# Kernel tuning notes

Hardware: AMD Instinct MI355X
Metric: run time of the kernel (lower is better)

Reference implementation:

```python
import jax, jax.numpy as jnp
import numpy as np

N_NODES = 10000
N_EDGES = 160000
T_STEPS = 2
N_SAMPLE = 2
H_DIM = 64
Z_DIM = 32
K_HEADS = 4
N_IN = 4


def setup_inputs() -> dict:
    key = jax.random.key(0)
    ks = jax.random.split(key, 16)
    sc = lambda fan_in: 1.0 / np.sqrt(fan_in).astype(np.float32)
    inp = {}
    inp["inputs"] = jax.random.normal(ks[0], (N_NODES, T_STEPS, N_IN), jnp.float32)
    inp["zA"] = jax.random.normal(ks[1], (N_NODES, N_SAMPLE, Z_DIM), jnp.float32)
    inp["zG"] = jax.random.normal(ks[2], (N_NODES, N_SAMPLE, Z_DIM), jnp.float32)
    inp["src"] = jax.random.randint(ks[3], (N_EDGES,), 0, N_NODES)
    inp["dst"] = jax.random.randint(ks[4], (N_EDGES,), 0, N_NODES)
    # GAT attention projections (K heads, no bias): Linear(z_dim -> h_dim)
    inp["Ws"] = jax.random.normal(ks[5], (K_HEADS, H_DIM, Z_DIM), jnp.float32) * sc(Z_DIM)
    inp["Wd"] = jax.random.normal(ks[6], (K_HEADS, H_DIM, Z_DIM), jnp.float32) * sc(Z_DIM)
    # F2: Linear(2h -> h, no bias), ReLU, Linear(h -> h, no bias)
    inp["F2_w1"] = jax.random.normal(ks[7], (H_DIM, 2 * H_DIM), jnp.float32) * sc(2 * H_DIM)
    inp["F2_w2"] = jax.random.normal(ks[8], (H_DIM, H_DIM), jnp.float32) * sc(H_DIM)
    # F1: Linear(K*h -> h, no bias), ReLU, Linear(h -> h, no bias)
    inp["F1_w1"] = jax.random.normal(ks[9], (H_DIM, K_HEADS * H_DIM), jnp.float32) * sc(K_HEADS * H_DIM)
    inp["F1_w2"] = jax.random.normal(ks[10], (H_DIM, H_DIM), jnp.float32) * sc(H_DIM)
    # x_enc: Linear(n_in -> h) with bias
    inp["xenc_w"] = jax.random.normal(ks[11], (H_DIM, N_IN), jnp.float32) * sc(N_IN)
    inp["xenc_b"] = jnp.zeros((H_DIM,), jnp.float32)
    # out_fc: Linear(h+z -> h), ReLU, Linear(h -> 4)
    inp["out_w1"] = jax.random.normal(ks[12], (H_DIM, H_DIM + Z_DIM), jnp.float32) * sc(H_DIM + Z_DIM)
    inp["out_b1"] = jnp.zeros((H_DIM,), jnp.float32)
    inp["out_w2"] = jax.random.normal(ks[13], (4, H_DIM), jnp.float32) * sc(H_DIM)
    inp["out_b2"] = jnp.zeros((4,), jnp.float32)
    inp["pred_steps"] = 2
    return inp


def reference(inputs, zA, zG, src, dst, Ws, Wd, F2_w1, F2_w2, F1_w1, F1_w2,
              xenc_w, xenc_b, out_w1, out_b1, out_w2, out_b2, pred_steps):
    N, T, _ = inputs.shape
    S = zA.shape[1]
    K = Ws.shape[0]

    # --- edge attention (GAT.attn), computed once per forward ---
    As = jnp.einsum('nsz,khz->nskh', zG, Ws)          # [N, S, K, H]
    Ad = jnp.einsum('nsz,khz->nskh', zG, Wd)
    e = jnp.sum(As[src] * Ad[dst], axis=-1)           # [E, S, K]
    e = jax.nn.leaky_relu(e, 0.01)
    # per-destination softmax over incoming edges (DGL mailbox softmax over dim=1)
    m = jax.ops.segment_max(e, dst, num_segments=N)
    ex = jnp.exp(e - m[dst])
    denom = jax.ops.segment_sum(ex, dst, num_segments=N)
    alpha = ex / denom[dst]                           # [E, S, K]
    deg = jax.ops.segment_sum(jnp.ones((e.shape[0],), e.dtype), dst, num_segments=N)
    deg = jnp.maximum(deg, 1.0)[:, None, None]        # [N, 1, 1]; mean over mailbox dim

    def step(xt):
        xt_enc = xt @ xenc_w.T + xenc_b               # [N, S, H]
        cat = jnp.concatenate([xt_enc[src], xt_enc[dst]], axis=-1)  # [E, S, 2H]
        dA = jax.nn.relu(cat @ F2_w1.T) @ F2_w2.T     # [E, S, H]
        # per-head attention-weighted mean over in-neighbors; loop over K (small, fixed)
        res = [jax.ops.segment_sum(alpha[:, :, k:k + 1] * dA, dst, num_segments=N) / deg
               for k in range(K)]
        res = jnp.concatenate(res, axis=-1)           # [N, S, K*H]
        deltax = jax.nn.relu(res @ F1_w1.T) @ F1_w2.T # [N, S, H]
        h = jnp.concatenate([deltax, zA], axis=-1)    # [N, S, H+Z]
        dx = jax.nn.relu(h @ out_w1.T + out_b1) @ out_w2.T + out_b2  # [N, S, 4]
        return xt + dx

    inp_t = jnp.transpose(inputs, (1, 0, 2))          # [T, N, n_in]
    inp_t = jnp.broadcast_to(inp_t[:, :, None, :], (T, N, S, inp_t.shape[-1]))
    preds = []
    for b in range(0, T, pred_steps):                 # blocks of pred_steps
        xt = inp_t[b]
        for _ in range(pred_steps):
            xt = step(xt)
            preds.append(xt)
    out = jnp.stack(preds, axis=0)                    # [T, N, S, 4]
    return jnp.transpose(out, (1, 0, 2, 3))           # [N, T, S, 4]
```

## Files before the change

### kernel.cpp

```cpp
#include <hip/hip_runtime.h>

#define NN 10000
#define NE 160000
#define TT 2
#define SS 2
#define HH 64
#define ZZ 32
#define KK 4
#define NIN 4

typedef short bf16x8 __attribute__((ext_vector_type(8)));
typedef float f32x4 __attribute__((ext_vector_type(4)));

__device__ __forceinline__ unsigned short f2b(float x) {
    unsigned u = __float_as_uint(x);
    u += 0x7fffu + ((u >> 16) & 1u);
    return (unsigned short)(u >> 16);
}
__device__ __forceinline__ float bf2f(unsigned short u) {
    return __uint_as_float(((unsigned)u) << 16);
}

__device__ __forceinline__ void wave_lds_fence() {
    asm volatile("s_waitcnt lgkmcnt(0)" ::: "memory");
    __builtin_amdgcn_wave_barrier();
}

__device__ __forceinline__ float edge_score(const unsigned* __restrict__ zp,
                                            const float* __restrict__ qf) {
    float a = 0.f;
#pragma unroll
    for (int j = 0; j < 16; ++j) {
        unsigned u = zp[j];
        a += __uint_as_float(u << 16) * qf[2*j]
           + __uint_as_float(u & 0xffff0000u) * qf[2*j+1];
    }
    return a > 0.f ? a : 0.01f*a;
}

__global__ __launch_bounds__(256) void k_prep(
    const float* __restrict__ Ws, const float* __restrict__ Wd,
    const float* __restrict__ F2w1, const float* __restrict__ xw,
    const float* __restrict__ xb, const float* __restrict__ F2w2,
    const float* __restrict__ F1w1, const float* __restrict__ F1w2,
    const float* __restrict__ ow1, const float* __restrict__ ow2,
    const float* __restrict__ zA, const float* __restrict__ zG,
    const float* __restrict__ inputs, const int* __restrict__ dst,
    float* __restrict__ MT, float* __restrict__ G1, float* __restrict__ G2,
    float* __restrict__ c1, float* __restrict__ c2,
    unsigned short* __restrict__ W2b, unsigned short* __restrict__ F1w1b,
    unsigned short* __restrict__ F1w2b, unsigned short* __restrict__ ow1b,
    unsigned short* __restrict__ ow2b, unsigned short* __restrict__ zAb,
    unsigned short* __restrict__ zGb, float* __restrict__ xt,
    int* __restrict__ deg_i)
{
    int b = blockIdx.x;
    int tid = threadIdx.x;
    if (b < 16) {
        int o = b*256 + tid;
        int j = o & 31, i = (o >> 5) & 31, k = o >> 10;
        float acc = 0.0f;
        for (int h = 0; h < HH; ++h)
            acc += Ws[(k*HH + h)*ZZ + i] * Wd[(k*HH + h)*ZZ + j];
        MT[(k*ZZ + j)*ZZ + i] = acc;
    } else if (b == 16) {
        int h = tid >> 2, i = tid & 3;
        float a1 = 0.f, a2 = 0.f;
        for (int j = 0; j < HH; ++j) {
            float x = xw[j*NIN + i];
            a1 += F2w1[h*128 + j] * x;
            a2 += F2w1[h*128 + 64 + j] * x;
        }
        G1[h*4 + i] = a1;
        G2[h*4 + i] = a2;
        if (i == 0) {
            float b1 = 0.f, b2 = 0.f;
            for (int j = 0; j < HH; ++j) {
                float bb = xb[j];
                b1 += F2w1[h*128 + j] * bb;
                b2 += F2w1[h*128 + 64 + j] * bb;
            }
            c1[h] = b1; c2[h] = b2;
        }
    } else {
        int t = (b - 17)*256 + tid;
        if (t < NN*SS*ZZ) { zAb[t] = f2b(zA[t]); zGb[t] = f2b(zG[t]); }
        if (t < HH*HH)    { W2b[t] = f2b(F2w2[t]); F1w2b[t] = f2b(F1w2[t]); }
        if (t < HH*KK*HH) F1w1b[t] = f2b(F1w1[t]);
        if (t < HH*(HH+ZZ)) ow1b[t] = f2b(ow1[t]);
        if (t < 4*HH)     ow2b[t] = f2b(ow2[t]);
        if (t < NN*SS*NIN) {
            int i = t & 3;
            int n = t >> 3;
            xt[t] = inputs[n*(TT*NIN) + i];
        }
        if (t < NE) atomicAdd(deg_i + dst[t], 1);
    }
}

__global__ void k_scan(const int* __restrict__ deg_i, int* __restrict__ offsets,
                       int* __restrict__ cursor) {
    __shared__ int buf0[1024], buf1[1024];
    int tidx = threadIdx.x;
    const int CH = (NN + 1023) / 1024;
    int b0 = tidx * CH;
    int sum = 0;
    for (int i = 0; i < CH; ++i) { int idx = b0 + i; if (idx < NN) sum += deg_i[idx]; }
    buf0[tidx] = sum;
    __syncthreads();
    int* s = buf0; int* d = buf1;
    for (int off = 1; off < 1024; off <<= 1) {
        d[tidx] = s[tidx] + (tidx >= off ? s[tidx - off] : 0);
        __syncthreads();
        int* tmp = s; s = d; d = tmp;
    }
    int run = s[tidx] - sum;
    for (int i = 0; i < CH; ++i) {
        int idx = b0 + i;
        if (idx < NN) { offsets[idx] = run; cursor[idx] = run; run += deg_i[idx]; }
    }
    if (tidx == 0) offsets[NN] = NE;
}

__global__ void k_scatter(const int* __restrict__ src, const int* __restrict__ dst,
                          int* __restrict__ cursor, int* __restrict__ src_by_pos) {
    int e = blockIdx.x * blockDim.x + threadIdx.x;
    if (e >= NE) return;
    int pos = atomicAdd(cursor + dst[e], 1);
    src_by_pos[pos] = src[e];
}

__global__ __launch_bounds__(64) void k_attn_agg0(
    const float* __restrict__ MT, const float* __restrict__ zG,
    const unsigned short* __restrict__ zGb, const int* __restrict__ src_by_pos,
    const int* __restrict__ offsets, const float* __restrict__ xt,
    const float* __restrict__ G1, const float* __restrict__ G2,
    const float* __restrict__ c1, const float* __restrict__ c2,
    float* alpha, unsigned short* __restrict__ agg_b)
{
    __shared__ float sq[132];
    __shared__ float alpha_s[64][4];
    int item = blockIdx.x;
    int n = item >> 1, s = item & 1;
    int l = threadIdx.x;
    int i = l >> 2, k = l & 3;
    int r0 = offsets[n], r1 = offsets[n+1];

    {
        int i0 = l & 31;
        int k0 = l >> 5;
        int k1 = k0 + 2;
        const float* zg = zG + item*ZZ;
        float acc0 = 0.f, acc1 = 0.f;
#pragma unroll
        for (int j = 0; j < ZZ; ++j) {
            float z = zg[j];
            acc0 += MT[(k0*ZZ + j)*ZZ + i0] * z;
            acc1 += MT[(k1*ZZ + j)*ZZ + i0] * z;
        }
        sq[k0*33 + i0] = acc0;
        sq[k1*33 + i0] = acc1;
    }
    wave_lds_fence();
    float qf[32];
#pragma unroll
    for (int j = 0; j < 32; ++j) qf[j] = sq[k*33 + j];

    float E[8];
    float mx = -1e30f;
    int nit = 0;
    for (int idx = r0 + i; idx < r1; idx += 16, ++nit) {
        int sn = src_by_pos[idx];
        float e = edge_score((const unsigned*)(zGb + (sn*SS + s)*ZZ), qf);
        if (nit < 8) E[nit] = e;
        mx = fmaxf(mx, e);
    }
#pragma unroll
    for (int off = 4; off < 64; off <<= 1) mx = fmaxf(mx, __shfl_xor(mx, off));
    float sum = 0.f;
    nit = 0;
    for (int idx = r0 + i; idx < r1; idx += 16, ++nit) {
        float e = (nit < 8) ? E[nit]
                : edge_score((const unsigned*)(zGb + (src_by_pos[idx]*SS + s)*ZZ), qf);
        float ex = __expf(e - mx);
        if (nit < 8) E[nit] = ex;
        sum += ex;
    }
#pragma unroll
    for (int off = 4; off < 64; off <<= 1) sum += __shfl_xor(sum, off);
    int deg = r1 - r0;
    float dd = (float)(deg > 1 ? deg : 1);
    float inv = sum > 0.f ? 1.f/(sum*dd) : 0.f;
    nit = 0;
    for (int idx = r0 + i; idx < r1; idx += 16, ++nit) {
        float a = ((nit < 8) ? E[nit]
                 : __expf(edge_score((const unsigned*)(zGb + (src_by_pos[idx]*SS + s)*ZZ), qf) - mx)) * inv;
        alpha[(idx*2 + s)*4 + k] = a;
        int jo = idx - r0;
        if (jo < 64) alpha_s[jo][k] = a;
    }
    wave_lds_fence();

    int h = l;
    const float4 g1 = *(const float4*)(G1 + h*4);
    const float4 g2 = *(const float4*)(G2 + h*4);
    const float4 xd = *(const float4*)(xt + item*4);
    float p2 = c2[h] + xd.x*g2.x + xd.y*g2.y + xd.z*g2.z + xd.w*g2.w;
    float c1h = c1[h];
    float a0 = 0.f, a1 = 0.f, a2 = 0.f, a3 = 0.f;
    int jo = 0;
    for (; jo + 4 <= deg; jo += 4) {
        int sn0 = src_by_pos[r0 + jo];
        int sn1 = src_by_pos[r0 + jo + 1];
        int sn2 = src_by_pos[r0 + jo + 2];
        int sn3 = src_by_pos[r0 + jo + 3];
        float4 x0 = *(const float4*)(xt + (sn0*SS + s)*NIN);
        float4 x1 = *(const float4*)(xt + (sn1*SS + s)*NIN);
        float4 x2 = *(const float4*)(xt + (sn2*SS + s)*NIN);
        float4 x3 = *(const float4*)(xt + (sn3*SS + s)*NIN);
        float4 w0 = (jo+0 < 64) ? *(const float4*)(&alpha_s[jo+0][0])
                                : *(const float4*)(alpha + ((r0+jo+0)*2 + s)*4);
        float4 w1 = (jo+1 < 64) ? *(const float4*)(&alpha_s[jo+1][0])
                                : *(const float4*)(alpha + ((r0+jo+1)*2 + s)*4);
        float4 w2 = (jo+2 < 64) ? *(const float4*)(&alpha_s[jo+2][0])
                                : *(const float4*)(alpha + ((r0+jo+2)*2 + s)*4);
        float4 w3 = (jo+3 < 64) ? *(const float4*)(&alpha_s[jo+3][0])
                                : *(const float4*)(alpha + ((r0+jo+3)*2 + s)*4);
        float p, hd;
        p = c1h + x0.x*g1.x + x0.y*g1.y + x0.z*g1.z + x0.w*g1.w;
        hd = p + p2; hd = hd > 0.f ? hd : 0.f;
        a0 += w0.x*hd; a1 += w0.y*hd; a2 += w0.z*hd; a3 += w0.w*hd;
        p = c1h + x1.x*g1.x + x1.y*g1.y + x1.z*g1.z + x1.w*g1.w;
        hd = p + p2; hd = hd > 0.f ? hd : 0.f;
        a0 += w1.x*hd; a1 += w1.y*hd; a2 += w1.z*hd; a3 += w1.w*hd;
        p = c1h + x2.x*g1.x + x2.y*g1.y + x2.z*g1.z + x2.w*g1.w;
        hd = p + p2; hd = hd > 0.f ? hd : 0.f;
        a0 += w2.x*hd; a1 += w2.y*hd; a2 += w2.z*hd; a3 += w2.w*hd;
        p = c1h + x3.x*g1.x + x3.y*g1.y + x3.z*g1.z + x3.w*g1.w;
        hd = p + p2; hd = hd > 0.f ? hd : 0.f;
        a0 += w3.x*hd; a1 += w3.y*hd; a2 += w3.z*hd; a3 += w3.w*hd;
    }
    for (; jo < deg; ++jo) {
        int sn = src_by_pos[r0 + jo];
        float4 x0 = *(const float4*)(xt + (sn*SS + s)*NIN);
        float4 w4 = (jo < 64) ? *(const float4*)(&alpha_s[jo][0])
                              : *(const float4*)(alpha + ((r0+jo)*2 + s)*4);
        float p = c1h + x0.x*g1.x + x0.y*g1.y + x0.z*g1.z + x0.w*g1.w;
        float hd = p + p2; hd = hd > 0.f ? hd : 0.f;
        a0 += w4.x*hd; a1 += w4.y*hd; a2 += w4.z*hd; a3 += w4.w*hd;
    }
    agg_b[item*256 +       h] = f2b(a0);
    agg_b[item*256 + 64  + h] = f2b(a1);
    agg_b[item*256 + 128 + h] = f2b(a2);
    agg_b[item*256 + 192 + h] = f2b(a3);
}

__global__ __launch_bounds__(64) void k_agg2(
    const float* __restrict__ xt, const float* __restrict__ G1,
    const float* __restrict__ G2, const float* __restrict__ c1,
    const float* __restrict__ c2, const int* __restrict__ src_by_pos,
    const int* __restrict__ offsets, const float* __restrict__ alpha,
    unsigned short* __restrict__ agg_b)
{
    int item = blockIdx.x;
    int n = item >> 1, s = item & 1;
    int h = threadIdx.x;
    int r0 = offsets[n], r1 = offsets[n+1];
    const float4 g1 = *(const float4*)(G1 + h*4);
    const float4 g2 = *(const float4*)(G2 + h*4);
    const float4 xd = *(const float4*)(xt + item*4);
    float p2 = c2[h] + xd.x*g2.x + xd.y*g2.y + xd.z*g2.z + xd.w*g2.w;
    float c1h = c1[h];
    float a0 = 0.f, a1 = 0.f, a2 = 0.f, a3 = 0.f;
    int idx = r0;
    for (; idx + 4 <= r1; idx += 4) {
        int sn0 = src_by_pos[idx];
        int sn1 = src_by_pos[idx+1];
        int sn2 = src_by_pos[idx+2];
        int sn3 = src_by_pos[idx+3];
        float4 x0 = *(const float4*)(xt + (sn0*SS + s)*NIN);
        float4 x1 = *(const float4*)(xt + (sn1*SS + s)*NIN);
        float4 x2 = *(const float4*)(xt + (sn2*SS + s)*NIN);
        float4 x3 = *(const float4*)(xt + (sn3*SS + s)*NIN);
        float4 w0 = *(const float4*)(alpha + ((idx+0)*2 + s)*4);
        float4 w1 = *(const float4*)(alpha + ((idx+1)*2 + s)*4);
        float4 w2 = *(const float4*)(alpha + ((idx+2)*2 + s)*4);
        float4 w3 = *(const float4*)(alpha + ((idx+3)*2 + s)*4);
        float p, hd;
        p = c1h + x0.x*g1.x + x0.y*g1.y + x0.z*g1.z + x0.w*g1.w;
        hd = p + p2; hd = hd > 0.f ? hd : 0.f;
        a0 += w0.x*hd; a1 += w0.y*hd; a2 += w0.z*hd; a3 += w0.w*hd;
        p = c1h + x1.x*g1.x + x1.y*g1.y + x1.z*g1.z + x1.w*g1.w;
        hd = p + p2; hd = hd > 0.f ? hd : 0.f;
        a0 += w1.x*hd; a1 += w1.y*hd; a2 += w1.z*hd; a3 += w1.w*hd;
        p = c1h + x2.x*g1.x + x2.y*g1.y + x2.z*g1.z + x2.w*g1.w;
        hd = p + p2; hd = hd > 0.f ? hd : 0.f;
        a0 += w2.x*hd; a1 += w2.y*hd; a2 += w2.z*hd; a3 += w2.w*hd;
        p = c1h + x3.x*g1.x + x3.y*g1.y + x3.z*g1.z + x3.w*g1.w;
        hd = p + p2; hd = hd > 0.f ? hd : 0.f;
        a0 += w3.x*hd; a1 += w3.y*hd; a2 += w3.z*hd; a3 += w3.w*hd;
    }
    for (; idx < r1; ++idx) {
        int sn = src_by_pos[idx];
        float4 x0 = *(const float4*)(xt + (sn*SS + s)*NIN);
        float4 w0 = *(const float4*)(alpha + (idx*2 + s)*4);
        float p = c1h + x0.x*g1.x + x0.y*g1.y + x0.z*g1.z + x0.w*g1.w;
        float hd = p + p2; hd = hd > 0.f ? hd : 0.f;
        a0 += w0.x*hd; a1 += w0.y*hd; a2 += w0.z*hd; a3 += w0.w*hd;
    }
    agg_b[item*256 +       h] = f2b(a0);
    agg_b[item*256 + 64  + h] = f2b(a1);
    agg_b[item*256 + 128 + h] = f2b(a2);
    agg_b[item*256 + 192 + h] = f2b(a3);
}

__global__ __launch_bounds__(256) void k_node_mfma(
    const unsigned short* __restrict__ agg_b, const unsigned short* __restrict__ zAb,
    const unsigned short* __restrict__ W2b,
    const unsigned short* __restrict__ F1w1b, const unsigned short* __restrict__ F1w2b,
    const unsigned short* __restrict__ ow1b, const unsigned short* __restrict__ ow2b,
    const float* __restrict__ ob1, const float* __restrict__ ob2,
    float* __restrict__ xt, float* __restrict__ out, int tstep)
{
    __shared__ unsigned short res_s[4][16*264];
    __shared__ unsigned short hid_s[4][16*72];
    __shared__ unsigned short hcat_s[4][16*104];
    int tid = threadIdx.x;
    int w = tid >> 6, l = tid & 63, l15 = l & 15, qq = l >> 4;

    bf16x8 w2f[2][4], b2f[2][4], o1f[3][4], bo2[2];
#pragma unroll
    for (int nb = 0; nb < 4; ++nb) {
        int n = nb*16 + l15;
#pragma unroll
        for (int kb = 0; kb < 2; ++kb) {
            w2f[kb][nb] = *(const bf16x8*)(W2b  + n*64 + kb*32 + qq*8);
            b2f[kb][nb] = *(const bf16x8*)(F1w2b + n*64 + kb*32 + qq*8);
        }
#pragma unroll
        for (int kb = 0; kb < 3; ++kb)
            o1f[kb][nb] = *(const bf16x8*)(ow1b + n*96 + kb*32 + qq*8);
    }
#pragma unroll
    for (int kb = 0; kb < 2; ++kb) {
        if (l15 < 4) bo2[kb] = *(const bf16x8*)(ow2b + l15*64 + kb*32 + qq*8);
        else {
            bf16x8 z;
#pragma unroll
            for (int j = 0; j < 8; ++j) z[j] = 0;
            bo2[kb] = z;
        }
    }
    float b1v[4];
#pragma unroll
    for (int nb = 0; nb < 4; ++nb) b1v[nb] = ob1[nb*16 + l15];
    float b2v = (l15 < 4) ? ob2[l15] : 0.0f;

    int itemBase = blockIdx.x*64 + w*16;
    if (itemBase >= NN*SS) return;

    *(uint4*)(&hcat_s[w][l15*104 + 64 + qq*8]) =
        *(const uint4*)(zAb + (itemBase + l15)*ZZ + qq*8);

#pragma unroll
    for (int k = 0; k < 4; ++k) {
        f32x4 acc0[4];
#pragma unroll
        for (int nb = 0; nb < 4; ++nb) acc0[nb] = (f32x4)(0.0f);
#pragma unroll
        for (int kb = 0; kb < 2; ++kb) {
            bf16x8 af = *(const bf16x8*)(agg_b + (itemBase + l15)*256 + k*64 + kb*32 + qq*8);
#pragma unroll
            for (int nb = 0; nb < 4; ++nb)
                acc0[nb] = __builtin_amdgcn_mfma_f32_16x16x32_bf16(af, w2f[kb][nb], acc0[nb], 0, 0, 0);
        }
#pragma unroll
        for (int nb = 0; nb < 4; ++nb)
#pragma unroll
            for (int r = 0; r < 4; ++r)
                res_s[w][(qq*4 + r)*264 + k*64 + nb*16 + l15] = f2b(acc0[nb][r]);
    }

    f32x4 acc[4];
#pragma unroll
    for (int nb = 0; nb < 4; ++nb) acc[nb] = (f32x4)(0.0f);
#pragma unroll
    for (int kb = 0; kb < 8; ++kb) {
        bf16x8 af = *(const bf16x8*)(&res_s[w][l15*264 + kb*32 + qq*8]);
#pragma unroll
        for (int nb = 0; nb < 4; ++nb) {
            bf16x8 bf = *(const bf16x8*)(F1w1b + (nb*16 + l15)*256 + kb*32 + qq*8);
            acc[nb] = __builtin_amdgcn_mfma_f32_16x16x32_bf16(af, bf, acc[nb], 0, 0, 0);
        }
    }
#pragma unroll
    for (int nb = 0; nb < 4; ++nb)
#pragma unroll
        for (int r = 0; r < 4; ++r) {
            float v = acc[nb][r];
            hid_s[w][(qq*4 + r)*72 + nb*16 + l15] = f2b(v > 0.0f ? v : 0.0f);
        }

    f32x4 acc2[4];
#pragma unroll
    for (int nb = 0; nb < 4; ++nb) acc2[nb] = (f32x4)(0.0f);
#pragma unroll
    for (int kb = 0; kb < 2; ++kb) {
        bf16x8 af = *(const bf16x8*)(&hid_s[w][l15*72 + kb*32 + qq*8]);
#pragma unroll
        for (int nb = 0; nb < 4; ++nb)
            acc2[nb] = __builtin_amdgcn_mfma_f32_16x16x32_bf16(af, b2f[kb][nb], acc2[nb], 0, 0, 0);
    }
#pragma unroll
    for (int nb = 0; nb < 4; ++nb)
#pragma unroll
        for (int r = 0; r < 4; ++r)
            hcat_s[w][(qq*4 + r)*104 + nb*16 + l15] = f2b(acc2[nb][r]);

    f32x4 acc3[4];
#pragma unroll
    for (int nb = 0; nb < 4; ++nb) acc3[nb] = (f32x4)(0.0f);
#pragma unroll
    for (int kb = 0; kb < 3; ++kb) {
        bf16x8 af = *(const bf16x8*)(&hcat_s[w][l15*104 + kb*32 + qq*8]);
#pragma unroll
        for (int nb = 0; nb < 4; ++nb)
            acc3[nb] = __builtin_amdgcn_mfma_f32_16x16x32_bf16(af, o1f[kb][nb], acc3[nb], 0, 0, 0);
    }
#pragma unroll
    for (int nb = 0; nb < 4; ++nb)
#pragma unroll
        for (int r = 0; r < 4; ++r) {
            float v = acc3[nb][r] + b1v[nb];
            hid_s[w][(qq*4 + r)*72 + nb*16 + l15] = f2b(v > 0.0f ? v : 0.0f);
        }

    f32x4 acc4 = (f32x4)(0.0f);
#pragma unroll
    for (int kb = 0; kb < 2; ++kb) {
        bf16x8 af = *(const bf16x8*)(&hid_s[w][l15*72 + kb*32 + qq*8]);
        acc4 = __builtin_amdgcn_mfma_f32_16x16x32_bf16(af, bo2[kb], acc4, 0, 0, 0);
    }
    if (l15 < 4) {
#pragma unroll
        for (int r = 0; r < 4; ++r) {
            int item = itemBase + qq*4 + r;
            float nx = xt[item*4 + l15] + acc4[r] + b2v;
            xt[item*4 + l15] = nx;
            int n = item >> 1, s = item & 1;
            out[((n*TT + tstep)*SS + s)*4 + l15] = nx;
        }
    }
}

extern "C" void kernel_launch(void* const* d_in, const int* in_sizes, int n_in,
                              void* d_out, int out_size, void* d_ws, size_t ws_size,
                              hipStream_t stream) {
    const float* inputs = (const float*)d_in[0];
    const float* zA     = (const float*)d_in[1];
    const float* zG     = (const float*)d_in[2];
    const int*   src    = (const int*)d_in[3];
    const int*   dst    = (const int*)d_in[4];
    const float* Ws     = (const float*)d_in[5];
    const float* Wd     = (const float*)d_in[6];
    const float* F2w1   = (const float*)d_in[7];
    const float* F2w2   = (const float*)d_in[8];
    const float* F1w1   = (const float*)d_in[9];
    const float* F1w2   = (const float*)d_in[10];
    const float* xw     = (const float*)d_in[11];
    const float* xb     = (const float*)d_in[12];
    const float* ow1    = (const float*)d_in[13];
    const float* ob1    = (const float*)d_in[14];
    const float* ow2    = (const float*)d_in[15];
    const float* ob2    = (const float*)d_in[16];
    float* out = (float*)d_out;

    float*          base        = (float*)d_ws;
    float*          MT          = base;
    float*          alpha       = base + 4096;
    int*            deg_i       = (int*)(base + 1284096);
    int*            offsets     = (int*)(base + 1294096);
    int*            cursor      = (int*)(base + 1304112);
    int*            src_by_pos  = (int*)(base + 1314112);
    float*          xt          = base + 1474112;
    float*          G1f         = base + 1554112;
    float*          G2f         = base + 1554368;
    float*          c1f         = base + 1554624;
    float*          c2f         = base + 1554688;
    unsigned short* W2b         = (unsigned short*)(base + 1554816);
    unsigned short* F1w1b       = (unsigned short*)(base + 1556864);
    unsigned short* F1w2b       = (unsigned short*)(base + 1565056);
    unsigned short* ow1b        = (unsigned short*)(base + 1567104);
    unsigned short* ow2b        = (unsigned short*)(base + 1570176);
    unsigned short* zAb         = (unsigned short*)(base + 1570304);
    unsigned short* zGb         = (unsigned short*)(base + 1890304);
    unsigned short* agg_b       = (unsigned short*)(base + 2210304);

    hipMemsetAsync(deg_i, 0, 10000u * 4u, stream);

    const int CONVB = (NN*SS*ZZ + 255)/256;
    k_prep<<<17 + CONVB, 256, 0, stream>>>(Ws, Wd, F2w1, xw, xb, F2w2, F1w1, F1w2,
                                           ow1, ow2, zA, zG, inputs, dst,
                                           MT, G1f, G2f, c1f, c2f,
                                           W2b, F1w1b, F1w2b, ow1b, ow2b,
                                           zAb, zGb, xt, deg_i);
    k_scan<<<1, 1024, 0, stream>>>(deg_i, offsets, cursor);
    k_scatter<<<(NE + 255)/256, 256, 0, stream>>>(src, dst, cursor, src_by_pos);

    k_attn_agg0<<<NN*SS, 64, 0, stream>>>(MT, zG, zGb, src_by_pos, offsets, xt,
                                          G1f, G2f, c1f, c2f, alpha, agg_b);
    k_node_mfma<<<(NN*SS + 63)/64, 256, 0, stream>>>(agg_b, zAb, W2b, F1w1b, F1w2b,
                                                     ow1b, ow2b, ob1, ob2, xt, out, 0);
    k_agg2<<<NN*SS, 64, 0, stream>>>(xt, G1f, G2f, c1f, c2f,
                                     src_by_pos, offsets, alpha, agg_b);
    k_node_mfma<<<(NN*SS + 63)/64, 256, 0, stream>>>(agg_b, zAb, W2b, F1w1b, F1w2b,
                                                     ow1b, ow2b, ob1, ob2, xt, out, 1);
}
```

Baseline: 226.7 us.

## Process both samples per node in one wave, halving block count

The attention and aggregation kernels now launch one 64-thread block per node instead of per (node, sample). Each half-wave handles one sample, and each lane computes two hidden channels. This shares the neighbor index loads across both samples and halves the number of blocks. In exchange, each lane does twice the per-edge arithmetic and the edge-score loops stride by 8 instead of 16, so high-degree nodes take more serial iterations.

```diff
diff --git a/kernel.cpp b/kernel.cpp
--- a/kernel.cpp
+++ b/kernel.cpp
@@ -138,48 +138,52 @@
     const float* __restrict__ c1, const float* __restrict__ c2,
     float* alpha, unsigned short* __restrict__ agg_b)
 {
-    __shared__ float sq[132];
-    __shared__ float alpha_s[64][4];
-    int item = blockIdx.x;
-    int n = item >> 1, s = item & 1;
+    __shared__ float sq[2][132];
+    __shared__ float alpha_s[2][64][4];
+    int n = blockIdx.x;
     int l = threadIdx.x;
-    int i = l >> 2, k = l & 3;
+    int half = l >> 5, hl = l & 31;
+    int s = half;
+    int item = n*2 + s;
+    int i = hl >> 2, k = hl & 3;
     int r0 = offsets[n], r1 = offsets[n+1];
+    int deg = r1 - r0;
 
     {
-        int i0 = l & 31;
-        int k0 = l >> 5;
-        int k1 = k0 + 2;
         const float* zg = zG + item*ZZ;
-        float acc0 = 0.f, acc1 = 0.f;
+        float acc0 = 0.f, acc1 = 0.f, acc2 = 0.f, acc3 = 0.f;
 #pragma unroll
         for (int j = 0; j < ZZ; ++j) {
             float z = zg[j];
-            acc0 += MT[(k0*ZZ + j)*ZZ + i0] * z;
-            acc1 += MT[(k1*ZZ + j)*ZZ + i0] * z;
-        }
-        sq[k0*33 + i0] = acc0;
-        sq[k1*33 + i0] = acc1;
+            acc0 += MT[(0*ZZ + j)*ZZ + hl] * z;
+            acc1 += MT[(1*ZZ + j)*ZZ + hl] * z;
+            acc2 += MT[(2*ZZ + j)*ZZ + hl] * z;
+            acc3 += MT[(3*ZZ + j)*ZZ + hl] * z;
+        }
+        sq[half][0*33 + hl] = acc0;
+        sq[half][1*33 + hl] = acc1;
+        sq[half][2*33 + hl] = acc2;
+        sq[half][3*33 + hl] = acc3;
     }
     wave_lds_fence();
     float qf[32];
 #pragma unroll
-    for (int j = 0; j < 32; ++j) qf[j] = sq[k*33 + j];
+    for (int j = 0; j < 32; ++j) qf[j] = sq[half][k*33 + j];
 
     float E[8];
     float mx = -1e30f;
     int nit = 0;
-    for (int idx = r0 + i; idx < r1; idx += 16, ++nit) {
+    for (int idx = r0 + i; idx < r1; idx += 8, ++nit) {
         int sn = src_by_pos[idx];
         float e = edge_score((const unsigned*)(zGb + (sn*SS + s)*ZZ), qf);
         if (nit < 8) E[nit] = e;
         mx = fmaxf(mx, e);
     }
 #pragma unroll
-    for (int off = 4; off < 64; off <<= 1) mx = fmaxf(mx, __shfl_xor(mx, off));
+    for (int off = 4; off < 32; off <<= 1) mx = fmaxf(mx, __shfl_xor(mx, off));
     float sum = 0.f;
     nit = 0;
-    for (int idx = r0 + i; idx < r1; idx += 16, ++nit) {
+    for (int idx = r0 + i; idx < r1; idx += 8, ++nit) {
         float e = (nit < 8) ? E[nit]
                 : edge_score((const unsigned*)(zGb + (src_by_pos[idx]*SS + s)*ZZ), qf);
         float ex = __expf(e - mx);
@@ -187,27 +191,30 @@
         sum += ex;
     }
 #pragma unroll
-    for (int off = 4; off < 64; off <<= 1) sum += __shfl_xor(sum, off);
-    int deg = r1 - r0;
+    for (int off = 4; off < 32; off <<= 1) sum += __shfl_xor(sum, off);
     float dd = (float)(deg > 1 ? deg : 1);
     float inv = sum > 0.f ? 1.f/(sum*dd) : 0.f;
     nit = 0;
-    for (int idx = r0 + i; idx < r1; idx += 16, ++nit) {
+    for (int idx = r0 + i; idx < r1; idx += 8, ++nit) {
         float a = ((nit < 8) ? E[nit]
                  : __expf(edge_score((const unsigned*)(zGb + (src_by_pos[idx]*SS + s)*ZZ), qf) - mx)) * inv;
         alpha[(idx*2 + s)*4 + k] = a;
         int jo = idx - r0;
-        if (jo < 64) alpha_s[jo][k] = a;
+        if (jo < 64) alpha_s[s][jo][k] = a;
     }
     wave_lds_fence();
 
-    int h = l;
-    const float4 g1 = *(const float4*)(G1 + h*4);
-    const float4 g2 = *(const float4*)(G2 + h*4);
+    int h = hl;
+    const float4 g1a = *(const float4*)(G1 + h*4);
+    const float4 g1b = *(const float4*)(G1 + (h+32)*4);
+    const float4 g2a = *(const float4*)(G2 + h*4);
+    const float4 g2b = *(const float4*)(G2 + (h+32)*4);
     const float4 xd = *(const float4*)(xt + item*4);
-    float p2 = c2[h] + xd.x*g2.x + xd.y*g2.y + xd.z*g2.z + xd.w*g2.w;
-    float c1h = c1[h];
+    float p2a = c2[h]    + xd.x*g2a.x + xd.y*g2a.y + xd.z*g2a.z + xd.w*g2a.w;
+    float p2b = c2[h+32] + xd.x*g2b.x + xd.y*g2b.y + xd.z*g2b.z + xd.w*g2b.w;
+    float c1a = c1[h], c1b = c1[h+32];
     float a0 = 0.f, a1 = 0.f, a2 = 0.f, a3 = 0.f;
+    float b0 = 0.f, b1 = 0.f, b2 = 0.f, b3 = 0.f;
     int jo = 0;
     for (; jo + 4 <= deg; jo += 4) {
         int sn0 = src_by_pos[r0 + jo];
@@ -218,41 +225,60 @@
         float4 x1 = *(const float4*)(xt + (sn1*SS + s)*NIN);
         float4 x2 = *(const float4*)(xt + (sn2*SS + s)*NIN);
         float4 x3 = *(const float4*)(xt + (sn3*SS + s)*NIN);
-        float4 w0 = (jo+0 < 64) ? *(const float4*)(&alpha_s[jo+0][0])
+        float4 w0 = (jo+0 < 64) ? *(const float4*)(&alpha_s[s][jo+0][0])
                                 : *(const float4*)(alpha + ((r0+jo+0)*2 + s)*4);
-        float4 w1 = (jo+1 < 64) ? *(const float4*)(&alpha_s[jo+1][0])
+        float4 w1 = (jo+1 < 64) ? *(const float4*)(&alpha_s[s][jo+1][0])
                                 : *(const float4*)(alpha + ((r0+jo+1)*2 + s)*4);
-        float4 w2 = (jo+2 < 64) ? *(const float4*)(&alpha_s[jo+2][0])
+        float4 w2 = (jo+2 < 64) ? *(const float4*)(&alpha_s[s][jo+2][0])
                                 : *(const float4*)(alpha + ((r0+jo+2)*2 + s)*4);
-        float4 w3 = (jo+3 < 64) ? *(const float4*)(&alpha_s[jo+3][0])
+        float4 w3 = (jo+3 < 64) ? *(const float4*)(&alpha_s[s][jo+3][0])
                                 : *(const float4*)(alpha + ((r0+jo+3)*2 + s)*4);
-        float p, hd;
-        p = c1h + x0.x*g1.x + x0.y*g1.y + x0.z*g1.z + x0.w*g1.w;
-        hd = p + p2; hd = hd > 0.f ? hd : 0.f;
-        a0 += w0.x*hd; a1 += w0.y*hd; a2 += w0.z*hd; a3 += w0.w*hd;
-        p = c1h + x1.x*g1.x + x1.y*g1.y + x1.z*g1.z + x1.w*g1.w;
-        hd = p + p2; hd = hd > 0.f ? hd : 0.f;
-        a0 += w1.x*hd; a1 += w1.y*hd; a2 += w1.z*hd; a3 += w1.w*hd;
-        p = c1h + x2.x*g1.x + x2.y*g1.y + x2.z*g1.z + x2.w*g1.w;
-        hd = p + p2; hd = hd > 0.f ? hd : 0.f;
-        a0 += w2.x*hd; a1 += w2.y*hd; a2 += w2.z*hd; a3 += w2.w*hd;
-        p = c1h + x3.x*g1.x + x3.y*g1.y + x3.z*g1.z + x3.w*g1.w;
-        hd = p + p2; hd = hd > 0.f ? hd : 0.f;
-        a0 += w3.x*hd; a1 += w3.y*hd; a2 += w3.z*hd; a3 += w3.w*hd;
+        float pa, pb, hda, hdb;
+        pa = c1a + x0.x*g1a.x + x0.y*g1a.y + x0.z*g1a.z + x0.w*g1a.w;
+        pb = c1b + x0.x*g1b.x + x0.y*g1b.y + x0.z*g1b.z + x0.w*g1b.w;
+        hda = pa + p2a; hda = hda > 0.f ? hda : 0.f;
+        hdb = pb + p2b; hdb = hdb > 0.f ? hdb : 0.f;
+        a0 += w0.x*hda; a1 += w0.y*hda; a2 += w0.z*hda; a3 += w0.w*hda;
+        b0 += w0.x*hdb; b1 += w0.y*hdb; b2 += w0.z*hdb; b3 += w0.w*hdb;
+        pa = c1a + x1.x*g1a.x + x1.y*g1a.y + x1.z*g1a.z + x1.w*g1a.w;
+        pb = c1b + x1.x*g1b.x + x1.y*g1b.y + x1.z*g1b.z + x1.w*g1b.w;
+        hda = pa + p2a; hda = hda > 0.f ? hda : 0.f;
+        hdb = pb + p2b; hdb = hdb > 0.f ? hdb : 0.f;
+        a0 += w1.x*hda; a1 += w1.y*hda; a2 += w1.z*hda; a3 += w1.w*hda;
+        b0 += w1.x*hdb; b1 += w1.y*hdb; b2 += w1.z*hdb; b3 += w1.w*hdb;
+        pa = c1a + x2.x*g1a.x + x2.y*g1a.y + x2.z*g1a.z + x2.w*g1a.w;
+        pb = c1b + x2.x*g1b.x + x2.y*g1b.y + x2.z*g1b.z + x2.w*g1b.w;
+        hda = pa + p2a; hda = hda > 0.f ? hda : 0.f;
+        hdb = pb + p2b; hdb = hdb > 0.f ? hdb : 0.f;
+        a0 += w2.x*hda; a1 += w2.y*hda; a2 += w2.z*hda; a3 += w2.w*hda;
+        b0 += w2.x*hdb; b1 += w2.y*hdb; b2 += w2.z*hdb; b3 += w2.w*hdb;
+        pa = c1a + x3.x*g1a.x + x3.y*g1a.y + x3.z*g1a.z + x3.w*g1a.w;
+        pb = c1b + x3.x*g1b.x + x3.y*g1b.y + x3.z*g1b.z + x3.w*g1b.w;
+        hda = pa + p2a; hda = hda > 0.f ? hda : 0.f;
+        hdb = pb + p2b; hdb = hdb > 0.f ? hdb : 0.f;
+        a0 += w3.x*hda; a1 += w3.y*hda; a2 += w3.z*hda; a3 += w3.w*hda;
+        b0 += w3.x*hdb; b1 += w3.y*hdb; b2 += w3.z*hdb; b3 += w3.w*hdb;
     }
     for (; jo < deg; ++jo) {
         int sn = src_by_pos[r0 + jo];
         float4 x0 = *(const float4*)(xt + (sn*SS + s)*NIN);
-        float4 w4 = (jo < 64) ? *(const float4*)(&alpha_s[jo][0])
+        float4 w4 = (jo < 64) ? *(const float4*)(&alpha_s[s][jo][0])
                               : *(const float4*)(alpha + ((r0+jo)*2 + s)*4);
-        float p = c1h + x0.x*g1.x + x0.y*g1.y + x0.z*g1.z + x0.w*g1.w;
-        float hd = p + p2; hd = hd > 0.f ? hd : 0.f;
-        a0 += w4.x*hd; a1 += w4.y*hd; a2 += w4.z*hd; a3 += w4.w*hd;
+        float pa = c1a + x0.x*g1a.x + x0.y*g1a.y + x0.z*g1a.z + x0.w*g1a.w;
+        float pb = c1b + x0.x*g1b.x + x0.y*g1b.y + x0.z*g1b.z + x0.w*g1b.w;
+        float hda = pa + p2a; hda = hda > 0.f ? hda : 0.f;
+        float hdb = pb + p2b; hdb = hdb > 0.f ? hdb : 0.f;
+        a0 += w4.x*hda; a1 += w4.y*hda; a2 += w4.z*hda; a3 += w4.w*hda;
+        b0 += w4.x*hdb; b1 += w4.y*hdb; b2 += w4.z*hdb; b3 += w4.w*hdb;
     }
     agg_b[item*256 +       h] = f2b(a0);
     agg_b[item*256 + 64  + h] = f2b(a1);
     agg_b[item*256 + 128 + h] = f2b(a2);
     agg_b[item*256 + 192 + h] = f2b(a3);
+    agg_b[item*256 +       h+32] = f2b(b0);
+    agg_b[item*256 + 64  + h+32] = f2b(b1);
+    agg_b[item*256 + 128 + h+32] = f2b(b2);
+    agg_b[item*256 + 192 + h+32] = f2b(b3);
 }
 
 __global__ __launch_bounds__(64) void k_agg2(
@@ -262,16 +288,23 @@
     const int* __restrict__ offsets, const float* __restrict__ alpha,
     unsigned short* __restrict__ agg_b)
 {
-    int item = blockIdx.x;
-    int n = item >> 1, s = item & 1;
-    int h = threadIdx.x;
+    int n = blockIdx.x;
+    int l = threadIdx.x;
+    int half = l >> 5, hl = l & 31;
+    int s = half;
+    int item = n*2 + s;
     int r0 = offsets[n], r1 = offsets[n+1];
-    const float4 g1 = *(const float4*)(G1 + h*4);
-    const float4 g2 = *(const float4*)(G2 + h*4);
+    int h = hl;
+    const float4 g1a = *(const float4*)(G1 + h*4);
+    const float4 g1b = *(const float4*)(G1 + (h+32)*4);
+    const float4 g2a = *(const float4*)(G2 + h*4);
+    const float4 g2b = *(const float4*)(G2 + (h+32)*4);
     const float4 xd = *(const float4*)(xt + item*4);
-    float p2 = c2[h] + xd.x*g2.x + xd.y*g2.y + xd.z*g2.z + xd.w*g2.w;
-    float c1h = c1[h];
+    float p2a = c2[h]    + xd.x*g2a.x + xd.y*g2a.y + xd.z*g2a.z + xd.w*g2a.w;
+    float p2b = c2[h+32] + xd.x*g2b.x + xd.y*g2b.y + xd.z*g2b.z + xd.w*g2b.w;
+    float c1a = c1[h], c1b = c1[h+32];
     float a0 = 0.f, a1 = 0.f, a2 = 0.f, a3 = 0.f;
+    float b0 = 0.f, b1 = 0.f, b2 = 0.f, b3 = 0.f;
     int idx = r0;
     for (; idx + 4 <= r1; idx += 4) {
         int sn0 = src_by_pos[idx];
@@ -286,32 +319,51 @@
         float4 w1 = *(const float4*)(alpha + ((idx+1)*2 + s)*4);
         float4 w2 = *(const float4*)(alpha + ((idx+2)*2 + s)*4);
         float4 w3 = *(const float4*)(alpha + ((idx+3)*2 + s)*4);
-        float p, hd;
-        p = c1h + x0.x*g1.x + x0.y*g1.y + x0.z*g1.z + x0.w*g1.w;
-        hd = p + p2; hd = hd > 0.f ? hd : 0.f;
-        a0 += w0.x*hd; a1 += w0.y*hd; a2 += w0.z*hd; a3 += w0.w*hd;
-        p = c1h + x1.x*g1.x + x1.y*g1.y + x1.z*g1.z + x1.w*g1.w;
-        hd = p + p2; hd = hd > 0.f ? hd : 0.f;
-        a0 += w1.x*hd; a1 += w1.y*hd; a2 += w1.z*hd; a3 += w1.w*hd;
-        p = c1h + x2.x*g1.x + x2.y*g1.y + x2.z*g1.z + x2.w*g1.w;
-        hd = p + p2; hd = hd > 0.f ? hd : 0.f;
-        a0 += w2.x*hd; a1 += w2.y*hd; a2 += w2.z*hd; a3 += w2.w*hd;
-        p = c1h + x3.x*g1.x + x3.y*g1.y + x3.z*g1.z + x3.w*g1.w;
-        hd = p + p2; hd = hd > 0.f ? hd : 0.f;
-        a0 += w3.x*hd; a1 += w3.y*hd; a2 += w3.z*hd; a3 += w3.w*hd;
+        float pa, pb, hda, hdb;
+        pa = c1a + x0.x*g1a.x + x0.y*g1a.y + x0.z*g1a.z + x0.w*g1a.w;
+        pb = c1b + x0.x*g1b.x + x0.y*g1b.y + x0.z*g1b.z + x0.w*g1b.w;
+        hda = pa + p2a; hda = hda > 0.f ? hda : 0.f;
+        hdb = pb + p2b; hdb = hdb > 0.f ? hdb : 0.f;
+        a0 += w0.x*hda; a1 += w0.y*hda; a2 += w0.z*hda; a3 += w0.w*hda;
+        b0 += w0.x*hdb; b1 += w0.y*hdb; b2 += w0.z*hdb; b3 += w0.w*hdb;
+        pa = c1a + x1.x*g1a.x + x1.y*g1a.y + x1.z*g1a.z + x1.w*g1a.w;
+        pb = c1b + x1.x*g1b.x + x1.y*g1b.y + x1.z*g1b.z + x1.w*g1b.w;
+        hda = pa + p2a; hda = hda > 0.f ? hda : 0.f;
+        hdb = pb + p2b; hdb = hdb > 0.f ? hdb : 0.f;
+        a0 += w1.x*hda; a1 += w1.y*hda; a2 += w1.z*hda; a3 += w1.w*hda;
+        b0 += w1.x*hdb; b1 += w1.y*hdb; b2 += w1.z*hdb; b3 += w1.w*hdb;
+        pa = c1a + x2.x*g1a.x + x2.y*g1a.y + x2.z*g1a.z + x2.w*g1a.w;
+        pb = c1b + x2.x*g1b.x + x2.y*g1b.y + x2.z*g1b.z + x2.w*g1b.w;
+        hda = pa + p2a; hda = hda > 0.f ? hda : 0.f;
+        hdb = pb + p2b; hdb = hdb > 0.f ? hdb : 0.f;
+        a0 += w2.x*hda; a1 += w2.y*hda; a2 += w2.z*hda; a3 += w2.w*hda;
+        b0 += w2.x*hdb; b1 += w2.y*hdb; b2 += w2.z*hdb; b3 += w2.w*hdb;
+        pa = c1a + x3.x*g1a.x + x3.y*g1a.y + x3.z*g1a.z + x3.w*g1a.w;
+        pb = c1b + x3.x*g1b.x + x3.y*g1b.y + x3.z*g1b.z + x3.w*g1b.w;
+        hda = pa + p2a; hda = hda > 0.f ? hda : 0.f;
+        hdb = pb + p2b; hdb = hdb > 0.f ? hdb : 0.f;
+        a0 += w3.x*hda; a1 += w3.y*hda; a2 += w3.z*hda; a3 += w3.w*hda;
+        b0 += w3.x*hdb; b1 += w3.y*hdb; b2 += w3.z*hdb; b3 += w3.w*hdb;
     }
     for (; idx < r1; ++idx) {
         int sn = src_by_pos[idx];
         float4 x0 = *(const float4*)(xt + (sn*SS + s)*NIN);
         float4 w0 = *(const float4*)(alpha + (idx*2 + s)*4);
-        float p = c1h + x0.x*g1.x + x0.y*g1.y + x0.z*g1.z + x0.w*g1.w;
-        float hd = p + p2; hd = hd > 0.f ? hd : 0.f;
-        a0 += w0.x*hd; a1 += w0.y*hd; a2 += w0.z*hd; a3 += w0.w*hd;
+        float pa = c1a + x0.x*g1a.x + x0.y*g1a.y + x0.z*g1a.z + x0.w*g1a.w;
+        float pb = c1b + x0.x*g1b.x + x0.y*g1b.y + x0.z*g1b.z + x0.w*g1b.w;
+        float hda = pa + p2a; hda = hda > 0.f ? hda : 0.f;
+        float hdb = pb + p2b; hdb = hdb > 0.f ? hdb : 0.f;
+        a0 += w0.x*hda; a1 += w0.y*hda; a2 += w0.z*hda; a3 += w0.w*hda;
+        b0 += w0.x*hdb; b1 += w0.y*hdb; b2 += w0.z*hdb; b3 += w0.w*hdb;
     }
     agg_b[item*256 +       h] = f2b(a0);
     agg_b[item*256 + 64  + h] = f2b(a1);
     agg_b[item*256 + 128 + h] = f2b(a2);
     agg_b[item*256 + 192 + h] = f2b(a3);
+    agg_b[item*256 +       h+32] = f2b(b0);
+    agg_b[item*256 + 64  + h+32] = f2b(b1);
+    agg_b[item*256 + 128 + h+32] = f2b(b2);
+    agg_b[item*256 + 192 + h+32] = f2b(b3);
 }
 
 __global__ __launch_bounds__(256) void k_node_mfma(
@@ -507,12 +559,12 @@
     k_scan<<<1, 1024, 0, stream>>>(deg_i, offsets, cursor);
     k_scatter<<<(NE + 255)/256, 256, 0, stream>>>(src, dst, cursor, src_by_pos);
 
-    k_attn_agg0<<<NN*SS, 64, 0, stream>>>(MT, zG, zGb, src_by_pos, offsets, xt,
-                                          G1f, G2f, c1f, c2f, alpha, agg_b);
+    k_attn_agg0<<<NN, 64, 0, stream>>>(MT, zG, zGb, src_by_pos, offsets, xt,
+                                       G1f, G2f, c1f, c2f, alpha, agg_b);
     k_node_mfma<<<(NN*SS + 63)/64, 256, 0, stream>>>(agg_b, zAb, W2b, F1w1b, F1w2b,
                                                      ow1b, ow2b, ob1, ob2, xt, out, 0);
-    k_agg2<<<NN*SS, 64, 0, stream>>>(xt, G1f, G2f, c1f, c2f,
-                                     src_by_pos, offsets, alpha, agg_b);
+    k_agg2<<<NN, 64, 0, stream>>>(xt, G1f, G2f, c1f, c2f,
+                                  src_by_pos, offsets, alpha, agg_b);
     k_node_mfma<<<(NN*SS + 63)/64, 256, 0, stream>>>(agg_b, zAb, W2b, F1w1b, F1w2b,
                                                      ow1b, ow2b, ob1, ob2, xt, out, 1);
 }
```

Result: no change. 223.2 us (-1.5%).
